# Kernel optimization log

Measured on AMD Instinct MI355X. Metric: run time of the kernel, lower is better.

Reference implementation:

```python
import jax, jax.numpy as jnp
from jax import lax
import numpy as np

N, T, HID, COMB, ATT, K, D = 128, 64, 512, 1024, 128, 20, 2
FMAP = 64  # CNN output channels; feature map is 14x14 -> 196 locations
ODIM = K + 2 * K * D + K + 1  # 121 mixture-density output params


def setup_inputs() -> dict:
    key = jax.random.key(0)
    keys = iter(jax.random.split(key, 64))

    def rn(shape, s=0.05):
        return jax.random.normal(next(keys), shape, jnp.float32) * s

    inp = dict(
        x=rn((N, T, D), 1.0),
        x_canv=jax.random.uniform(next(keys), (N, 1, 28, 28), dtype=jnp.float32),
        start=rn((N, D), 1.0),
        conv1_w=rn((16, 1, 3, 3), 0.3), conv1_b=rn((16,)),
        conv2_w=rn((32, 16, 3, 3), 0.1), conv2_b=rn((32,)),
        conv3_w=rn((64, 32, 3, 3), 0.1), conv3_b=rn((64,)),
        init_w=rn((2 * HID, FMAP + 16)), init_b=rn((2 * HID,)),
        Uw=rn((ATT, HID)), Ub=rn((ATT,)),
        Ww=rn((ATT, FMAP)), Wb=rn((ATT,)),
        vw=rn((1, ATT)), vb=rn((1,)),
        beta_w=rn((FMAP, HID)), beta_b=rn((FMAP,)),
        xemb_w=rn((16, D), 0.5), xemb_b=rn((16,)),
        semb_w=rn((16, D), 0.5), semb_b=rn((16,)),
        Wih=rn((4 * HID, FMAP + 16)), Whh=rn((4 * HID, HID)),
        bih=rn((4 * HID,)), bhh=rn((4 * HID,)),
        comb_w=rn((COMB, FMAP + HID + 32)), comb_b=rn((COMB,)),
        out_w=rn((ODIM, COMB)), out_b=rn((ODIM,)),
    )
    return inp


def _conv(x, w, b, stride):
    # torch Conv2d(kernel=3, padding=1) with NCHW / OIHW layout
    y = lax.conv_general_dilated(x, w, (stride, stride), ((1, 1), (1, 1)),
                                 dimension_numbers=('NCHW', 'OIHW', 'NCHW'))
    return y + b[None, :, None, None]


def reference(x, x_canv, start, conv1_w, conv1_b, conv2_w, conv2_b, conv3_w, conv3_b,
              init_w, init_b, Uw, Ub, Ww, Wb, vw, vb, beta_w, beta_b,
              xemb_w, xemb_b, semb_w, semb_b, Wih, Whh, bih, bhh,
              comb_w, comb_b, out_w, out_b):
    n, Tt, d = x.shape
    # sequence_pad: prepend zero vector, drop last step
    xp = jnp.concatenate([jnp.zeros((n, 1, d), x.dtype), x[:, :-1]], axis=1)
    xe = jnp.tanh(xp @ xemb_w.T + xemb_b)          # (n,T,16)
    se = jnp.tanh(start @ semb_w.T + semb_b)       # (n,16)
    # CNN (zscore_canvases with new_stats=True)
    c = (x_canv - 0.0243) / 0.1383
    c = jax.nn.relu(_conv(c, conv1_w, conv1_b, 1))
    c = jax.nn.relu(_conv(c, conv2_w, conv2_b, 1))
    c = jnp.tanh(_conv(c, conv3_w, conv3_b, 2))    # (n,64,14,14)
    a = c.transpose(0, 2, 3, 1).reshape(n, -1, FMAP)  # (n,196,64)
    # Initialize LSTM state (num_layers=1)
    hidden = jnp.tanh(jnp.concatenate([a.mean(axis=1), se], axis=1) @ init_w.T + init_b)
    hidden = hidden.reshape(n, HID, 2)
    h0, c0 = hidden[:, :, 0], hidden[:, :, 1]
    # AttendSAT.register_annotation: precompute W(a)
    W_a = a @ Ww.T + Wb                             # (n,196,att)
    # dropout masks are keep-probs (eval / dropout=0) -> all ones, identity

    def step(carry, xt):
        h, cs = carry
        Uh = h @ Uw.T + Ub                          # (n,att)
        e = (jnp.tanh(W_a + Uh[:, None, :]) @ vw.T).squeeze(-1) + vb[0]
        alpha = jax.nn.softmax(e, axis=-1)          # (n,196)
        z = jnp.einsum('nlf,nl->nf', a, alpha)      # (n,64)
        z = jax.nn.sigmoid(h @ beta_w.T + beta_b) * z
        gates = jnp.concatenate([xt, z], axis=1) @ Wih.T + bih + h @ Whh.T + bhh
        gi, gf, gg, go = jnp.split(gates, 4, axis=1)  # torch gate order i,f,g,o
        cs = jax.nn.sigmoid(gf) * cs + jax.nn.sigmoid(gi) * jnp.tanh(gg)
        h = jax.nn.sigmoid(go) * jnp.tanh(cs)
        y = jnp.tanh(jnp.concatenate([h, z, xt, se], axis=1) @ comb_w.T + comb_b)
        y = y @ out_w.T + out_b
        return (h, cs), y

    _, ys = lax.scan(step, (h0, c0), xe.transpose(1, 0, 2))
    y_out = ys.transpose(1, 0, 2)                   # (n,T,121)
    # unpack_output
    mix, means, scales, corrs, vlog = jnp.split(
        y_out, [K, K + K * D, K + 2 * K * D, 2 * K + 2 * K * D], axis=-1)
    mix = jax.nn.softmax(mix, axis=-1)
    means = means.reshape(n, Tt, K, D)
    scales = jnp.exp(scales).reshape(n, Tt, K, D)
    corrs = jnp.tanh(corrs)
    return (mix, means, scales, corrs, vlog.squeeze(-1))
```

## Files before the change

### kernel.cpp

```cpp
#include <hip/hip_runtime.h>


#define TN 128
#define TT 64

typedef __attribute__((ext_vector_type(4))) float f32x4;
typedef __attribute__((ext_vector_type(8))) short bf16x8;

__device__ __forceinline__ float fsigm(float x){ return __builtin_amdgcn_rcpf(1.0f + __expf(-x)); }
__device__ __forceinline__ float ftanh(float x){ return 1.0f - 2.0f*__builtin_amdgcn_rcpf(1.0f + __expf(2.0f*x)); }
__device__ __forceinline__ unsigned short f2bf(float f){
  unsigned int u = __float_as_uint(f);
  u += 0x7fffu + ((u >> 16) & 1u);
  return (unsigned short)(u >> 16);
}
__device__ __forceinline__ float b2f(unsigned short u){ return __uint_as_float(((unsigned)u)<<16); }

__global__ __launch_bounds__(256) void k_conv1(const float* __restrict__ xc, const float* __restrict__ w,
                                               const float* __restrict__ b, float* __restrict__ c1){
  int idx = blockIdx.x*256 + threadIdx.x;
  if (idx >= TN*16*784) return;
  int p = idx % 784, oc = (idx/784) & 15, n = idx/(784*16);
  int py = p/28, px = p%28;
  const float* src = xc + n*784;
  float acc = b[oc];
  #pragma unroll
  for (int ky=0;ky<3;ky++){
    int iy = py+ky-1; if (iy<0||iy>=28) continue;
    #pragma unroll
    for (int kx=0;kx<3;kx++){
      int ix = px+kx-1; if (ix<0||ix>=28) continue;
      acc += (src[iy*28+ix]-0.0243f)*(1.0f/0.1383f) * w[oc*9+ky*3+kx];
    }
  }
  c1[idx] = fmaxf(acc, 0.0f);
}

__global__ __launch_bounds__(256) void k_im2col2(const float* __restrict__ c1, unsigned short* __restrict__ a2){
  int idx = blockIdx.x*256 + threadIdx.x;
  int k = idx % 160, r = idx / 160;
  unsigned short v = 0;
  if (k < 144){
    int ic = k/9, rem = k - ic*9, ky = rem/3, kx = rem - ky*3;
    int p = r % 784, n = r / 784;
    int py = p/28, px = p%28;
    int iy = py+ky-1, ix = px+kx-1;
    if (iy>=0 && iy<28 && ix>=0 && ix<28) v = f2bf(c1[(n*16+ic)*784 + iy*28+ix]);
  }
  a2[idx] = v;
}

__global__ __launch_bounds__(256) void k_gconv2(const unsigned short* __restrict__ a2,
    const unsigned short* __restrict__ w2b, const float* __restrict__ b2,
    unsigned short* __restrict__ c2bf){
  int mbase = blockIdx.x*128;
  int tid = threadIdx.x, w = tid>>6, l = tid&63;
  int lr = l&15, lk = (l>>4)*8;
  __shared__ unsigned short at[128*168];
  {
    int row = tid>>1, off = (tid&1)*80;
    const unsigned short* sp = a2 + (size_t)(mbase+row)*160 + off;
    #pragma unroll
    for (int j=0;j<10;j++) *(float4*)&at[row*168 + off + j*8] = *(const float4*)(sp + j*8);
  }
  __syncthreads();
  f32x4 acc[2][2];
  #pragma unroll
  for (int mi=0;mi<2;mi++){ acc[mi][0]=(f32x4){0,0,0,0}; acc[mi][1]=(f32x4){0,0,0,0}; }
  for (int kt=0; kt<5; ++kt){
    bf16x8 b0 = *(const bf16x8*)(w2b + (0*16+lr)*160 + kt*32 + lk);
    bf16x8 b1 = *(const bf16x8*)(w2b + (1*16+lr)*160 + kt*32 + lk);
    #pragma unroll
    for (int mi=0;mi<2;mi++){
      bf16x8 afrag = *(const bf16x8*)&at[((2*w+mi)*16+lr)*168 + kt*32 + lk];
      acc[mi][0] = __builtin_amdgcn_mfma_f32_16x16x32_bf16(afrag, b0, acc[mi][0], 0,0,0);
      acc[mi][1] = __builtin_amdgcn_mfma_f32_16x16x32_bf16(afrag, b1, acc[mi][1], 0,0,0);
    }
  }
  #pragma unroll
  for (int mi=0;mi<2;mi++){
    #pragma unroll
    for (int j=0;j<2;j++){
      int oc = j*16 + lr;
      float bb = b2[oc];
      #pragma unroll
      for (int i=0;i<4;i++){
        int r = mbase + (2*w+mi)*16 + (l>>4)*4 + i;
        c2bf[(size_t)r*32 + oc] = f2bf(fmaxf(acc[mi][j][i] + bb, 0.0f));
      }
    }
  }
}

__global__ __launch_bounds__(256) void k_im2col3(const unsigned short* __restrict__ c2bf, unsigned short* __restrict__ a3){
  int idx = blockIdx.x*256 + threadIdx.x;
  int k = idx % 320, r = idx / 320;
  unsigned short v = 0;
  if (k < 288){
    int ic = k/9, rem = k - ic*9, ky = rem/3, kx = rem - ky*3;
    int p = r % 196, n = r / 196;
    int py = p/14, px = p%14;
    int iy = 2*py+ky-1, ix = 2*px+kx-1;
    if (iy>=0 && iy<28 && ix>=0 && ix<28) v = c2bf[(size_t)(n*784 + iy*28+ix)*32 + ic];
  }
  a3[idx] = v;
}

__global__ __launch_bounds__(256) void k_gconv3(const unsigned short* __restrict__ a3,
    const unsigned short* __restrict__ w3b, const float* __restrict__ b3,
    unsigned short* __restrict__ afbf, unsigned short* __restrict__ abf){
  int mbase = blockIdx.x*128;
  int tid = threadIdx.x, w = tid>>6, l = tid&63;
  int lr = l&15, lk = (l>>4)*8;
  __shared__ unsigned short at[128*168];
  f32x4 acc[2][4];
  #pragma unroll
  for (int mi=0;mi<2;mi++)
    #pragma unroll
    for (int j=0;j<4;j++) acc[mi][j]=(f32x4){0,0,0,0};
  for (int kt2=0; kt2<2; ++kt2){
    {
      int row = tid>>1, off = (tid&1)*80;
      const unsigned short* sp = a3 + (size_t)(mbase+row)*320 + kt2*160 + off;
      #pragma unroll
      for (int j=0;j<10;j++) *(float4*)&at[row*168 + off + j*8] = *(const float4*)(sp + j*8);
    }
    __syncthreads();
    for (int kt=0; kt<5; ++kt){
      #pragma unroll
      for (int mi=0;mi<2;mi++){
        bf16x8 afrag = *(const bf16x8*)&at[((2*w+mi)*16+lr)*168 + kt*32 + lk];
        #pragma unroll
        for (int j=0;j<4;j++){
          bf16x8 bf = *(const bf16x8*)(w3b + (size_t)(j*16+lr)*320 + kt2*160 + kt*32 + lk);
          acc[mi][j] = __builtin_amdgcn_mfma_f32_16x16x32_bf16(afrag, bf, acc[mi][j], 0,0,0);
        }
      }
    }
    __syncthreads();
  }
  #pragma unroll
  for (int mi=0;mi<2;mi++){
    #pragma unroll
    for (int j=0;j<4;j++){
      int oc = j*16 + lr;
      float bb = b3[oc];
      #pragma unroll
      for (int i=0;i<4;i++){
        int r = mbase + (2*w+mi)*16 + (l>>4)*4 + i;
        int n = r/196, p = r - n*196;
        float v = ftanh(acc[mi][j][i] + bb);
        unsigned short vb16 = f2bf(v);
        afbf[(size_t)(n*64+oc)*196 + p] = vb16;
        abf[(size_t)r*64 + oc] = vb16;
      }
    }
  }
}

__global__ __launch_bounds__(64) void k_amean(const unsigned short* __restrict__ afbf, float* __restrict__ amean){
  int n = blockIdx.x, f = threadIdx.x;
  const unsigned short* row = afbf + (size_t)(n*64+f)*196;
  float s = 0;
  for (int l=0;l<196;l++) s += b2f(row[l]);
  amean[n*64+f] = s * (1.0f/196.0f);
}

__global__ __launch_bounds__(256) void k_embed(const float* __restrict__ x, const float* __restrict__ start,
    const float* __restrict__ xw, const float* __restrict__ xb,
    const float* __restrict__ sw, const float* __restrict__ sb,
    float* __restrict__ xe, float* __restrict__ se){
  int idx = blockIdx.x*256 + threadIdx.x;
  if (idx < TN*TT*16){
    int j = idx & 15, t = (idx>>4) & 63, n = idx>>10;
    float acc = xb[j];
    if (t > 0){
      const float* xp = x + (n*TT + t-1)*2;
      acc += xp[0]*xw[j*2] + xp[1]*xw[j*2+1];
    }
    xe[idx] = ftanh(acc);
  } else if (idx < TN*TT*16 + TN*16){
    int k2 = idx - TN*TT*16;
    int j = k2 & 15, n = k2 >> 4;
    float acc = sb[j] + start[n*2]*sw[j*2] + start[n*2+1]*sw[j*2+1];
    se[k2] = ftanh(acc);
  }
}

__global__ __launch_bounds__(256) void k_init(const float* __restrict__ amean, const float* __restrict__ se,
    const float* __restrict__ w, const float* __restrict__ b,
    unsigned short* __restrict__ hbfA, float* __restrict__ cbuf){
  int idx = blockIdx.x*256 + threadIdx.x;
  if (idx >= TN*1024) return;
  int o = idx & 1023, n = idx >> 10;
  const float* wr = w + o*80;
  float acc = b[o];
  for (int k2=0;k2<64;k2++) acc += amean[n*64+k2]*wr[k2];
  for (int k2=0;k2<16;k2++) acc += se[n*16+k2]*wr[64+k2];
  float v = ftanh(acc);
  if (o & 1) cbuf[n*512 + (o>>1)] = v;
  else       hbfA[n*512 + (o>>1)] = f2bf(v);
}

__global__ __launch_bounds__(256) void k_prep(
    const float* __restrict__ Whh, const float* __restrict__ Wih,
    const float* __restrict__ bih, const float* __restrict__ bhh,
    const float* __restrict__ comb_w, const float* __restrict__ out_w, const float* __restrict__ out_b,
    const float* __restrict__ Uw, const float* __restrict__ beta_w, const float* __restrict__ Ww,
    const float* __restrict__ conv2_w, const float* __restrict__ conv3_w,
    unsigned short* __restrict__ wgf, float* __restrict__ gbias,
    unsigned short* __restrict__ cwbf, unsigned short* __restrict__ owbf, float* __restrict__ obias,
    unsigned short* __restrict__ uwbf, unsigned short* __restrict__ betabf, unsigned short* __restrict__ wwbf,
    unsigned short* __restrict__ w2b, unsigned short* __restrict__ w3b){
  int idx = blockIdx.x*256 + threadIdx.x;
  if (idx < 1245184){
    int fragi = idx >> 9;
    int lane8 = idx & 511;
    int lane = lane8 >> 3, j = lane8 & 7;
    int g = fragi / 608;
    int rem = fragi - g*608;
    int b = rem / 19, kt = rem - b*19;
    int row = g*512 + b*16 + (lane & 15);
    int col = kt*32 + (lane >> 4)*8 + j;
    float v = 0.f;
    if (col < 512) v = Whh[(size_t)row*512 + col];
    else { int c2 = col - 512; if (c2 < 80) v = Wih[(size_t)row*80 + c2]; }
    wgf[idx] = f2bf(v);
    return;
  }
  idx -= 1245184;
  if (idx < 2048){ gbias[idx] = bih[idx]+bhh[idx]; return; }
  idx -= 2048;
  if (idx < 622592){ cwbf[idx] = f2bf(comb_w[idx]); return; }
  idx -= 622592;
  if (idx < 131072){ int o = idx>>10, k2 = idx & 1023; owbf[idx] = (o<121)? f2bf(out_w[o*1024+k2]) : (unsigned short)0; return; }
  idx -= 131072;
  if (idx < 128){ obias[idx] = (idx<121)? out_b[idx] : 0.0f; return; }
  idx -= 128;
  if (idx < 65536){ uwbf[idx] = f2bf(Uw[idx]); return; }
  idx -= 65536;
  if (idx < 32768){ betabf[idx] = f2bf(beta_w[idx]); return; }
  idx -= 32768;
  if (idx < 8192){ wwbf[idx] = f2bf(Ww[idx]); return; }
  idx -= 8192;
  if (idx < 5120){ int o = idx/160, k2 = idx - o*160; w2b[idx] = (k2<144)? f2bf(conv2_w[o*144+k2]) : (unsigned short)0; return; }
  idx -= 5120;
  if (idx < 20480){ int o = idx/320, k2 = idx - o*320; w3b[idx] = (k2<288)? f2bf(conv3_w[o*320-o*320+o*320]) : (unsigned short)0;  }
  if (idx < 20480){ int o = idx/320, k2 = idx - o*320; w3b[idx] = (k2<288)? f2bf(conv3_w[o*288+k2]) : (unsigned short)0; return; }
}

__global__ __launch_bounds__(256) void k_wa(const unsigned short* __restrict__ abf,
    const unsigned short* __restrict__ wwbf, const float* __restrict__ Wb,
    unsigned short* __restrict__ wabf){
  int mbase = blockIdx.x*128;
  int tid = threadIdx.x, w = tid>>6, l = tid&63;
  int lr = l & 15, lk = (l>>4)*8;
  __shared__ unsigned short at[128*40];
  f32x4 acc[8][2];
  #pragma unroll
  for (int m=0;m<8;m++){ acc[m][0] = (f32x4){0,0,0,0}; acc[m][1] = (f32x4){0,0,0,0}; }
  for (int kt=0; kt<2; ++kt){
    int row = tid>>1, half = (tid&1)*16;
    const unsigned short* sp = abf + (mbase+row)*64 + kt*32 + half;
    *(float4*)&at[row*40 + half]     = *(const float4*)sp;
    *(float4*)&at[row*40 + half + 8] = *(const float4*)(sp + 8);
    __syncthreads();
    bf16x8 b0 = *(const bf16x8*)(wwbf + ((2*w+0)*16 + lr)*64 + kt*32 + lk);
    bf16x8 b1 = *(const bf16x8*)(wwbf + ((2*w+1)*16 + lr)*64 + kt*32 + lk);
    #pragma unroll
    for (int m=0;m<8;m++){
      bf16x8 afrag = *(const bf16x8*)&at[(m*16+lr)*40 + lk];
      acc[m][0] = __builtin_amdgcn_mfma_f32_16x16x32_bf16(afrag, b0, acc[m][0], 0,0,0);
      acc[m][1] = __builtin_amdgcn_mfma_f32_16x16x32_bf16(afrag, b1, acc[m][1], 0,0,0);
    }
    __syncthreads();
  }
  #pragma unroll
  for (int m=0;m<8;m++){
    #pragma unroll
    for (int j=0;j<2;j++){
      int att = (2*w+j)*16 + lr;
      float wb = Wb[att];
      #pragma unroll
      for (int i=0;i<4;i++){
        int arow = mbase + m*16 + (l>>4)*4 + i;
        int n = arow/196, l2 = arow - n*196;
        wabf[((size_t)n*196 + l2)*128 + att] = f2bf(acc[m][j][i] + wb);
      }
    }
  }
}

__global__ __launch_bounds__(512) void k_stepA(int t,
    const unsigned short* __restrict__ hbf_in,
    const unsigned short* __restrict__ uwbf, const float* __restrict__ Ub,
    const unsigned short* __restrict__ betabf, const float* __restrict__ beta_b,
    const float* __restrict__ vw, const float* __restrict__ vb,
    const unsigned short* __restrict__ wabf, const unsigned short* __restrict__ afbf,
    unsigned short* __restrict__ ubf_all, unsigned short* __restrict__ cbf,
    const unsigned short* __restrict__ wgf, float* __restrict__ gpart)
{
  const int bid = blockIdx.x, tid = threadIdx.x;
  __shared__ __align__(16) float hs[512];
  __shared__ __align__(16) float Uh[128];
  __shared__ __align__(16) float vws[128];
  __shared__ float bsig[64];
  __shared__ float ew[196];
  __shared__ float red[16];
  __shared__ float up[4][128];
  __shared__ float qp8[8][64];
  __shared__ float ep2[256][2];
  __shared__ __align__(16) unsigned short at2[2][128*36];

  if (bid < TN){
    const int n = bid;
    hs[tid] = b2f(hbf_in[n*512 + tid]);
    if (tid < 128) vws[tid] = vw[tid];
    const float vb0 = vb[0];
    __syncthreads();
    {
      int att = tid & 127, q = tid >> 7;
      const unsigned short* uw = uwbf + (size_t)att*512 + q*128;
      const float* hh = hs + q*128;
      float acc = 0.f;
      #pragma unroll 4
      for (int k=0;k<128;k+=8){
        bf16x8 v = *(const bf16x8*)(uw + k);
        acc += hh[k+0]*b2f(v[0]) + hh[k+1]*b2f(v[1]) + hh[k+2]*b2f(v[2]) + hh[k+3]*b2f(v[3])
             + hh[k+4]*b2f(v[4]) + hh[k+5]*b2f(v[5]) + hh[k+6]*b2f(v[6]) + hh[k+7]*b2f(v[7]);
      }
      up[q][att] = acc;
    }
    {
      int f = tid & 63, q = tid >> 6;
      const unsigned short* bw = betabf + (size_t)f*512 + q*64;
      const float* hh = hs + q*64;
      float acc = 0.f;
      #pragma unroll 4
      for (int k=0;k<64;k+=8){
        bf16x8 v = *(const bf16x8*)(bw + k);
        acc += hh[k+0]*b2f(v[0]) + hh[k+1]*b2f(v[1]) + hh[k+2]*b2f(v[2]) + hh[k+3]*b2f(v[3])
             + hh[k+4]*b2f(v[4]) + hh[k+5]*b2f(v[5]) + hh[k+6]*b2f(v[6]) + hh[k+7]*b2f(v[7]);
      }
      qp8[q][f] = acc;
    }
    __syncthreads();
    if (tid < 128) Uh[tid] = Ub[tid] + up[0][tid]+up[1][tid]+up[2][tid]+up[3][tid];
    else if (tid < 192){
      int f = tid-128;
      bsig[f] = fsigm(beta_b[f] + qp8[0][f]+qp8[1][f]+qp8[2][f]+qp8[3][f]
                                + qp8[4][f]+qp8[5][f]+qp8[6][f]+qp8[7][f]);
    }
    __syncthreads();
    {
      int l = tid >> 1, half = tid & 1;
      float acc = 0.f;
      if (l < 196){
        const unsigned short* wr = wabf + ((size_t)n*196 + l)*128 + half*64;
        const float* uh = Uh + half*64;
        const float* vv = vws + half*64;
        #pragma unroll 2
        for (int k=0;k<64;k+=8){
          bf16x8 wv = *(const bf16x8*)(wr + k);
          acc += vv[k+0]*ftanh(b2f(wv[0]) + uh[k+0]) + vv[k+1]*ftanh(b2f(wv[1]) + uh[k+1])
               + vv[k+2]*ftanh(b2f(wv[2]) + uh[k+2]) + vv[k+3]*ftanh(b2f(wv[3]) + uh[k+3])
               + vv[k+4]*ftanh(b2f(wv[4]) + uh[k+4]) + vv[k+5]*ftanh(b2f(wv[5]) + uh[k+5])
               + vv[k+6]*ftanh(b2f(wv[6]) + uh[k+6]) + vv[k+7]*ftanh(b2f(wv[7]) + uh[k+7]);
        }
      }
      ep2[l][half] = acc;
    }
    __syncthreads();
    float ev = -1e30f;
    if (tid < 196) ev = vb0 + ep2[tid][0] + ep2[tid][1];
    float m = ev;
    #pragma unroll
    for (int off=32; off>0; off>>=1) m = fmaxf(m, __shfl_xor(m, off));
    if ((tid&63)==0) red[tid>>6] = m;
    __syncthreads();
    float mx = red[0];
    #pragma unroll
    for (int i=1;i<8;i++) mx = fmaxf(mx, red[i]);
    float ex = (tid<196) ? __expf(ev - mx) : 0.0f;
    float ss = ex;
    #pragma unroll
    for (int off=32; off>0; off>>=1) ss += __shfl_xor(ss, off);
    if ((tid&63)==0) red[8+(tid>>6)] = ss;
    if (tid<196) ew[tid] = ex;
    __syncthreads();
    float inv = __builtin_amdgcn_rcpf(red[8]+red[9]+red[10]+red[11]+red[12]+red[13]+red[14]+red[15]);
    {
      int f = tid & 63, q = tid >> 6;
      int l0 = q*25, l1 = (l0+25 < 196) ? l0+25 : 196;
      const unsigned short* an = afbf + (size_t)n*12544 + (size_t)f*196;
      float acc = 0.f;
      for (int l2=l0; l2<l1; l2++) acc += ew[l2]*b2f(an[l2]);
      qp8[q][f] = acc;
    }
    __syncthreads();
    if (tid < 64){
      float z = bsig[tid]*(qp8[0][tid]+qp8[1][tid]+qp8[2][tid]+qp8[3][tid]
                          +qp8[4][tid]+qp8[5][tid]+qp8[6][tid]+qp8[7][tid])*inv;
      unsigned short zb = f2bf(z);
      ubf_all[((size_t)t*TN + n)*96 + 16 + tid] = zb;
      cbf[((size_t)n*TT + t)*608 + 512 + tid] = zb;
    }
  } else {
    const int b = bid - TN;
    const int w = tid>>6, l = tid&63, lr = l&15, li = l>>4, lk = li*8;
    const int g = w & 3, mh = w >> 2;
    bf16x8 wreg[16];
    {
      const unsigned short* wp = wgf + ((size_t)(g*32 + b)*19)*512 + (size_t)l*8;
      #pragma unroll
      for (int i=0;i<16;i++) wreg[i] = *(const bf16x8*)(wp + (size_t)i*512);
    }
    f32x4 acc[4];
    #pragma unroll
    for (int m2=0;m2<4;m2++) acc[m2] = (f32x4){0,0,0,0};
    {
      int row = tid>>2, seg = (tid&3)*8;
      *(float4*)&at2[0][row*36+seg] = *(const float4*)(hbf_in + (size_t)row*512 + seg);
    }
    __syncthreads();
    for (int kt=0; kt<16; ++kt){
      if (kt+1 < 16){
        int row = tid>>2, seg = (tid&3)*8;
        *(float4*)&at2[(kt+1)&1][row*36+seg] = *(const float4*)(hbf_in + (size_t)row*512 + (kt+1)*32 + seg);
      }
      #pragma unroll
      for (int m2=0;m2<4;m2++){
        bf16x8 a = *(const bf16x8*)&at2[kt&1][((mh*4+m2)*16 + lr)*36 + lk];
        acc[m2] = __builtin_amdgcn_mfma_f32_16x16x32_bf16(a, wreg[kt], acc[m2], 0,0,0);
      }
      __syncthreads();
    }
    #pragma unroll
    for (int m2=0;m2<4;m2++){
      #pragma unroll
      for (int i=0;i<4;i++){
        int n2 = (mh*4+m2)*16 + li*4 + i;
        gpart[(((size_t)g*128 + n2)<<9) + b*16 + lr] = acc[m2][i];
      }
    }
  }
}

__global__ __launch_bounds__(256) void k_stepB(int t,
    unsigned short* __restrict__ hout,
    const unsigned short* __restrict__ ubf_all,
    const unsigned short* __restrict__ wgf, const float* __restrict__ gbias,
    const float* __restrict__ gpart,
    float* __restrict__ cbuf, unsigned short* __restrict__ cbf)
{
  const int b = blockIdx.x, tid = threadIdx.x;
  const int w = tid>>6, l = tid&63, lr = l&15, li = l>>4, lk = li*8;
  __shared__ float gsh[4][128][16];
  __shared__ __align__(16) unsigned short at[128*100];
  const unsigned short* ub = ubf_all + (size_t)t*TN*96;
  for (int i = tid; i < 2048; i += 256){
    int g = i>>9, r = i&511, n2 = r>>2, j4 = r&3;
    *(float4*)&gsh[g][n2][j4*4] = *(const float4*)&gpart[(((size_t)g*128 + n2)<<9) + b*16 + j4*4];
  }
  for (int i = tid; i < 1536; i += 256){
    int row = i/12, c8 = i - row*12;
    *(float4*)&at[row*100 + c8*8] = *(const float4*)(ub + (size_t)row*96 + c8*8);
  }
  bf16x8 wz[3];
  {
    const unsigned short* wp = wgf + (((size_t)(w*32 + b)*19) + 16)*512 + (size_t)l*8;
    #pragma unroll
    for (int i=0;i<3;i++) wz[i] = *(const bf16x8*)(wp + (size_t)i*512);
  }
  f32x4 acc[8];
  #pragma unroll
  for (int m=0;m<8;m++) acc[m] = (f32x4){0,0,0,0};
  __syncthreads();
  #pragma unroll
  for (int kt=0; kt<3; ++kt){
    #pragma unroll
    for (int m=0;m<8;m++){
      bf16x8 a = *(const bf16x8*)&at[(m*16+lr)*100 + kt*32 + lk];
      acc[m] = __builtin_amdgcn_mfma_f32_16x16x32_bf16(a, wz[kt], acc[m], 0,0,0);
    }
  }
  #pragma unroll
  for (int m=0;m<8;m++)
    #pragma unroll
    for (int i=0;i<4;i++)
      gsh[w][m*16 + li*4 + i][lr] += acc[m][i];
  __syncthreads();
  #pragma unroll
  for (int e=0;e<8;++e){
    int c = tid*8 + e;
    int nn = c>>4, j = c&15;
    int hidx = b*16 + j;
    float gi = gsh[0][nn][j] + gbias[         hidx];
    float gf = gsh[1][nn][j] + gbias[1*512 + hidx];
    float gg = gsh[2][nn][j] + gbias[2*512 + hidx];
    float go = gsh[3][nn][j] + gbias[3*512 + hidx];
    float cc = cbuf[nn*512 + hidx];
    float cs = fsigm(gf)*cc + fsigm(gi)*ftanh(gg);
    float h  = fsigm(go)*ftanh(cs);
    cbuf[nn*512 + hidx] = cs;
    unsigned short hb = f2bf(h);
    hout[nn*512 + hidx] = hb;
    cbf[((size_t)nn*TT + t)*608 + hidx] = hb;
  }
}

__global__ __launch_bounds__(256) void k_cbf_xs(const float* __restrict__ xe, const float* __restrict__ se,
                                                unsigned short* __restrict__ cbf,
                                                unsigned short* __restrict__ ubf_all){
  int idx = blockIdx.x*256 + threadIdx.x;
  if (idx >= TN*TT*64) return;
  int j = idx & 63, r = idx >> 6;
  int n = r >> 6, t = r & 63;
  if (j < 16)      cbf[(size_t)r*608 + 576 + j] = f2bf(xe[r*16 + j]);
  else if (j < 32) cbf[(size_t)r*608 + 592 + (j-16)] = f2bf(se[n*16 + (j-16)]);
  else if (j < 48) ubf_all[((size_t)t*TN + n)*96 + (j-32)] = f2bf(xe[r*16 + (j-32)]);
  else             ubf_all[((size_t)t*TN + n)*96 + 80 + (j-48)] = 0;
}

__global__ __launch_bounds__(256) void k_comb(const unsigned short* __restrict__ cbf,
    const unsigned short* __restrict__ cwbf, const float* __restrict__ comb_b,
    unsigned short* __restrict__ ybf){
  int mbase = blockIdx.x*128, obase = blockIdx.y*128;
  int tid = threadIdx.x, w = tid>>6, l = tid&63;
  int lr = l&15, lk = (l>>4)*8;
  __shared__ unsigned short at[128*40];
  f32x4 acc[8][2];
  #pragma unroll
  for (int m=0;m<8;m++){ acc[m][0] = (f32x4){0,0,0,0}; acc[m][1] = (f32x4){0,0,0,0}; }
  for (int kt=0; kt<19; ++kt){
    int row = tid>>1, half = (tid&1)*16;
    const unsigned short* sp = cbf + (size_t)(mbase+row)*608 + kt*32 + half;
    *(float4*)&at[row*40 + half]     = *(const float4*)sp;
    *(float4*)&at[row*40 + half + 8] = *(const float4*)(sp + 8);
    __syncthreads();
    bf16x8 b0 = *(const bf16x8*)(cwbf + (size_t)(obase + (2*w+0)*16 + lr)*608 + kt*32 + lk);
    bf16x8 b1 = *(const bf16x8*)(cwbf + (size_t)(obase + (2*w+1)*16 + lr)*608 + kt*32 + lk);
    #pragma unroll
    for (int m=0;m<8;m++){
      bf16x8 afrag = *(const bf16x8*)&at[(m*16+lr)*40 + lk];
      acc[m][0] = __builtin_amdgcn_mfma_f32_16x16x32_bf16(afrag, b0, acc[m][0], 0,0,0);
      acc[m][1] = __builtin_amdgcn_mfma_f32_16x16x32_bf16(afrag, b1, acc[m][1], 0,0,0);
    }
    __syncthreads();
  }
  #pragma unroll
  for (int m=0;m<8;m++){
    #pragma unroll
    for (int j=0;j<2;j++){
      int o = obase + (2*w+j)*16 + lr;
      float cb = comb_b[o];
      #pragma unroll
      for (int i=0;i<4;i++){
        int r = mbase + m*16 + (l>>4)*4 + i;
        ybf[(size_t)r*1024 + o] = f2bf(ftanh(acc[m][j][i] + cb));
      }
    }
  }
}

__global__ __launch_bounds__(256) void k_out(const unsigned short* __restrict__ ybf,
    const unsigned short* __restrict__ owbf, const float* __restrict__ obias,
    float* __restrict__ obuf){
  int mbase = blockIdx.x*128;
  int tid = threadIdx.x, w = tid>>6, l = tid&63;
  int lr = l&15, lk = (l>>4)*8;
  __shared__ unsigned short at[128*40];
  f32x4 acc[8][2];
  #pragma unroll
  for (int m=0;m<8;m++){ acc[m][0] = (f32x4){0,0,0,0}; acc[m][1] = (f32x4){0,0,0,0}; }
  for (int kt=0; kt<32; ++kt){
    int row = tid>>1, half = (tid&1)*16;
    const unsigned short* sp = ybf + (size_t)(mbase+row)*1024 + kt*32 + half;
    *(float4*)&at[row*40 + half]     = *(const float4*)sp;
    *(float4*)&at[row*40 + half + 8] = *(const float4*)(sp + 8);
    __syncthreads();
    bf16x8 b0 = *(const bf16x8*)(owbf + ((2*w+0)*16 + lr)*1024 + kt*32 + lk);
    bf16x8 b1 = *(const bf16x8*)(owbf + ((2*w+1)*16 + lr)*1024 + kt*32 + lk);
    #pragma unroll
    for (int m=0;m<8;m++){
      bf16x8 afrag = *(const bf16x8*)&at[(m*16+lr)*40 + lk];
      acc[m][0] = __builtin_amdgcn_mfma_f32_16x16x32_bf16(afrag, b0, acc[m][0], 0,0,0);
      acc[m][1] = __builtin_amdgcn_mfma_f32_16x16x32_bf16(afrag, b1, acc[m][1], 0,0,0);
    }
    __syncthreads();
  }
  #pragma unroll
  for (int m=0;m<8;m++){
    #pragma unroll
    for (int j=0;j<2;j++){
      int o = (2*w+j)*16 + lr;
      float ob = obias[o];
      #pragma unroll
      for (int i=0;i<4;i++){
        int r = mbase + m*16 + (l>>4)*4 + i;
        obuf[(size_t)r*128 + o] = acc[m][j][i] + ob;
      }
    }
  }
}

__global__ __launch_bounds__(256) void k_post(const float* __restrict__ obuf, float* __restrict__ out){
  int r = blockIdx.x*256 + threadIdx.x;
  if (r >= TN*TT) return;
  const float* row = obuf + (size_t)r*128;
  float mx = -1e30f;
  #pragma unroll
  for (int k2=0;k2<20;k2++) mx = fmaxf(mx, row[k2]);
  float e[20]; float s = 0;
  #pragma unroll
  for (int k2=0;k2<20;k2++){ e[k2] = __expf(row[k2]-mx); s += e[k2]; }
  float inv = __builtin_amdgcn_rcpf(s);
  float* mixo  = out;
  float* meano = out + 163840;
  float* scaleo= out + 491520;
  float* corro = out + 819200;
  float* vlogo = out + 983040;
  #pragma unroll
  for (int k2=0;k2<20;k2++) mixo[r*20+k2] = e[k2]*inv;
  #pragma unroll
  for (int j=0;j<40;j++) meano[r*40+j] = row[20+j];
  #pragma unroll
  for (int j=0;j<40;j++) scaleo[r*40+j] = __expf(row[60+j]);
  #pragma unroll
  for (int k2=0;k2<20;k2++) corro[r*20+k2] = ftanh(row[100+k2]);
  vlogo[r] = row[120];
}

extern "C" void kernel_launch(void* const* d_in, const int* in_sizes, int n_in,
                              void* d_out, int out_size, void* d_ws, size_t ws_size,
                              hipStream_t stream){
  const float* x       = (const float*)d_in[0];
  const float* x_canv  = (const float*)d_in[1];
  const float* start_  = (const float*)d_in[2];
  const float* conv1_w = (const float*)d_in[3];
  const float* conv1_b = (const float*)d_in[4];
  const float* conv2_w = (const float*)d_in[5];
  const float* conv2_b = (const float*)d_in[6];
  const float* conv3_w = (const float*)d_in[7];
  const float* conv3_b = (const float*)d_in[8];
  const float* init_w  = (const float*)d_in[9];
  const float* init_b  = (const float*)d_in[10];
  const float* Uw      = (const float*)d_in[11];
  const float* Ub      = (const float*)d_in[12];
  const float* Ww      = (const float*)d_in[13];
  const float* Wb      = (const float*)d_in[14];
  const float* vw      = (const float*)d_in[15];
  const float* vb      = (const float*)d_in[16];
  const float* beta_w  = (const float*)d_in[17];
  const float* beta_b  = (const float*)d_in[18];
  const float* xemb_w  = (const float*)d_in[19];
  const float* xemb_b  = (const float*)d_in[20];
  const float* semb_w  = (const float*)d_in[21];
  const float* semb_b  = (const float*)d_in[22];
  const float* Wih     = (const float*)d_in[23];
  const float* Whh     = (const float*)d_in[24];
  const float* bih     = (const float*)d_in[25];
  const float* bhh     = (const float*)d_in[26];
  const float* comb_w  = (const float*)d_in[27];
  const float* comb_b  = (const float*)d_in[28];
  const float* out_w   = (const float*)d_in[29];
  const float* out_b   = (const float*)d_in[30];
  (void)in_sizes; (void)n_in; (void)out_size; (void)ws_size;

  char* wsb = (char*)d_ws;
  size_t off = 0;
  auto alloc = [&](size_t bytes)->char*{
    char* p = wsb + off;
    off = (off + bytes + 255) & ~(size_t)255;
    return p;
  };
  float*          c1     = (float*)alloc((size_t)TN*16*784*4);
  unsigned short* a2     = (unsigned short*)alloc((size_t)100352*160*2);
  unsigned short* a3     = a2;
  unsigned short* c2bf   = (unsigned short*)alloc((size_t)100352*32*2);
  unsigned short* afbf   = (unsigned short*)alloc((size_t)TN*64*196*2);
  unsigned short* abf    = (unsigned short*)alloc((size_t)TN*196*64*2);
  float*          amean  = (float*)alloc((size_t)TN*64*4);
  float*          xe     = (float*)alloc((size_t)TN*TT*16*4);
  float*          se     = (float*)alloc((size_t)TN*16*4);
  unsigned short* wabf   = (unsigned short*)alloc((size_t)TN*196*128*2);
  float*          cbuf   = (float*)alloc((size_t)TN*512*4);
  unsigned short* hbfA   = (unsigned short*)alloc((size_t)TN*512*2);
  unsigned short* hbfB   = (unsigned short*)alloc((size_t)TN*512*2);
  unsigned short* ubf_all= (unsigned short*)alloc((size_t)TT*TN*96*2);
  unsigned short* cbf    = (unsigned short*)alloc((size_t)TN*TT*608*2);
  unsigned short* ybf    = (unsigned short*)alloc((size_t)TN*TT*1024*2);
  float*          obuf   = (float*)alloc((size_t)TN*TT*128*4);
  unsigned short* wgf    = (unsigned short*)alloc((size_t)1245184*2);
  float*          gbias  = (float*)alloc((size_t)2048*4);
  float*          gpart  = (float*)alloc((size_t)4*128*512*4);
  unsigned short* cwbf   = (unsigned short*)alloc((size_t)1024*608*2);
  unsigned short* owbf   = (unsigned short*)alloc((size_t)128*1024*2);
  float*          obias  = (float*)alloc((size_t)128*4);
  unsigned short* uwbf   = (unsigned short*)alloc((size_t)128*512*2);
  unsigned short* betabf = (unsigned short*)alloc((size_t)64*512*2);
  unsigned short* wwbf   = (unsigned short*)alloc((size_t)128*64*2);
  unsigned short* w2b    = (unsigned short*)alloc((size_t)32*160*2);
  unsigned short* w3b    = (unsigned short*)alloc((size_t)64*320*2);

  hipLaunchKernelGGL(k_conv1, dim3(6272), dim3(256), 0, stream, x_canv, conv1_w, conv1_b, c1);
  hipLaunchKernelGGL(k_prep, dim3(8334), dim3(256), 0, stream,
                     Whh, Wih, bih, bhh, comb_w, out_w, out_b, Uw, beta_w, Ww, conv2_w, conv3_w,
                     wgf, gbias, cwbf, owbf, obias, uwbf, betabf, wwbf, w2b, w3b);
  hipLaunchKernelGGL(k_im2col2, dim3(62720), dim3(256), 0, stream, c1, a2);
  hipLaunchKernelGGL(k_gconv2, dim3(784), dim3(256), 0, stream, a2, w2b, conv2_b, c2bf);
  hipLaunchKernelGGL(k_im2col3, dim3(31360), dim3(256), 0, stream, c2bf, a3);
  hipLaunchKernelGGL(k_gconv3, dim3(196), dim3(256), 0, stream, a3, w3b, conv3_b, afbf, abf);
  hipLaunchKernelGGL(k_amean, dim3(128), dim3(64), 0, stream, afbf, amean);
  hipLaunchKernelGGL(k_embed, dim3(520), dim3(256), 0, stream, x, start_, xemb_w, xemb_b, semb_w, semb_b, xe, se);
  hipLaunchKernelGGL(k_init, dim3(512), dim3(256), 0, stream, amean, se, init_w, init_b, hbfA, cbuf);
  hipLaunchKernelGGL(k_wa, dim3(196), dim3(256), 0, stream, abf, wwbf, Wb, wabf);
  hipLaunchKernelGGL(k_cbf_xs, dim3(2048), dim3(256), 0, stream, xe, se, cbf, ubf_all);

  for (int t = 0; t < TT; ++t){
    unsigned short* hin  = (t & 1) ? hbfB : hbfA;
    unsigned short* hout = (t & 1) ? hbfA : hbfB;
    hipLaunchKernelGGL(k_stepA, dim3(160), dim3(512), 0, stream, t,
                       hin, uwbf, Ub, betabf, beta_b, vw, vb, wabf, afbf, ubf_all, cbf, wgf, gpart);
    hipLaunchKernelGGL(k_stepB, dim3(32), dim3(256), 0, stream, t,
                       hout, ubf_all, wgf, gbias, gpart, cbuf, cbf);
  }

  hipLaunchKernelGGL(k_comb, dim3(64, 8), dim3(256), 0, stream, cbf, cwbf, comb_b, ybf);
  hipLaunchKernelGGL(k_out, dim3(64), dim3(256), 0, stream, ybf, owbf, obias, obuf);
  hipLaunchKernelGGL(k_post, dim3(32), dim3(256), 0, stream, obuf, (float*)d_out);
}
```

Before: 1.670 ms.

## Store conv1 as bf16, read MFMA operands from global, widen stepB to 512 threads

conv1 now writes its output as bf16, which halves the traffic into im2col2 and drops a conversion there. In the recurrent kernels, the MFMA A operand (h and the u inputs) is loaded straight from global memory instead of being staged through double-buffered shared memory, which removes the per-iteration barriers. k_stepB goes from 256 to 512 threads, so each wave covers half the rows, following the same split as stepA's gate blocks. A stray duplicate store in the weight-prep kernel is also removed. The direct global loads depend on L2 and cache hits and are less coalesced than the staged path.

New measurement: 2.193 ms. +31.4%, slower.

```diff
diff --git a/kernel.cpp b/kernel.cpp
--- a/kernel.cpp
+++ b/kernel.cpp
@@ -17,7 +17,7 @@
 __device__ __forceinline__ float b2f(unsigned short u){ return __uint_as_float(((unsigned)u)<<16); }
 
 __global__ __launch_bounds__(256) void k_conv1(const float* __restrict__ xc, const float* __restrict__ w,
-                                               const float* __restrict__ b, float* __restrict__ c1){
+                                               const float* __restrict__ b, unsigned short* __restrict__ c1bf){
   int idx = blockIdx.x*256 + threadIdx.x;
   if (idx >= TN*16*784) return;
   int p = idx % 784, oc = (idx/784) & 15, n = idx/(784*16);
@@ -33,10 +33,10 @@
       acc += (src[iy*28+ix]-0.0243f)*(1.0f/0.1383f) * w[oc*9+ky*3+kx];
     }
   }
-  c1[idx] = fmaxf(acc, 0.0f);
-}
-
-__global__ __launch_bounds__(256) void k_im2col2(const float* __restrict__ c1, unsigned short* __restrict__ a2){
+  c1bf[idx] = f2bf(fmaxf(acc, 0.0f));
+}
+
+__global__ __launch_bounds__(256) void k_im2col2(const unsigned short* __restrict__ c1bf, unsigned short* __restrict__ a2){
   int idx = blockIdx.x*256 + threadIdx.x;
   int k = idx % 160, r = idx / 160;
   unsigned short v = 0;
@@ -45,7 +45,7 @@
     int p = r % 784, n = r / 784;
     int py = p/28, px = p%28;
     int iy = py+ky-1, ix = px+kx-1;
-    if (iy>=0 && iy<28 && ix>=0 && ix<28) v = f2bf(c1[(n*16+ic)*784 + iy*28+ix]);
+    if (iy>=0 && iy<28 && ix>=0 && ix<28) v = c1bf[(n*16+ic)*784 + iy*28+ix];
   }
   a2[idx] = v;
 }
@@ -245,7 +245,6 @@
   idx -= 8192;
   if (idx < 5120){ int o = idx/160, k2 = idx - o*160; w2b[idx] = (k2<144)? f2bf(conv2_w[o*144+k2]) : (unsigned short)0; return; }
   idx -= 5120;
-  if (idx < 20480){ int o = idx/320, k2 = idx - o*320; w3b[idx] = (k2<288)? f2bf(conv3_w[o*320-o*320+o*320]) : (unsigned short)0;  }
   if (idx < 20480){ int o = idx/320, k2 = idx - o*320; w3b[idx] = (k2<288)? f2bf(conv3_w[o*288+k2]) : (unsigned short)0; return; }
 }
 
@@ -310,7 +309,6 @@
   __shared__ float up[4][128];
   __shared__ float qp8[8][64];
   __shared__ float ep2[256][2];
-  __shared__ __align__(16) unsigned short at2[2][128*36];
 
   if (bid < TN){
     const int n = bid;
@@ -418,22 +416,13 @@
     f32x4 acc[4];
     #pragma unroll
     for (int m2=0;m2<4;m2++) acc[m2] = (f32x4){0,0,0,0};
-    {
-      int row = tid>>2, seg = (tid&3)*8;
-      *(float4*)&at2[0][row*36+seg] = *(const float4*)(hbf_in + (size_t)row*512 + seg);
-    }
-    __syncthreads();
+    #pragma unroll 4
     for (int kt=0; kt<16; ++kt){
-      if (kt+1 < 16){
-        int row = tid>>2, seg = (tid&3)*8;
-        *(float4*)&at2[(kt+1)&1][row*36+seg] = *(const float4*)(hbf_in + (size_t)row*512 + (kt+1)*32 + seg);
-      }
       #pragma unroll
       for (int m2=0;m2<4;m2++){
-        bf16x8 a = *(const bf16x8*)&at2[kt&1][((mh*4+m2)*16 + lr)*36 + lk];
+        bf16x8 a = *(const bf16x8*)(hbf_in + (size_t)((mh*4+m2)*16 + lr)*512 + kt*32 + lk);
         acc[m2] = __builtin_amdgcn_mfma_f32_16x16x32_bf16(a, wreg[kt], acc[m2], 0,0,0);
       }
-      __syncthreads();
     }
     #pragma unroll
     for (int m2=0;m2<4;m2++){
@@ -446,7 +435,7 @@
   }
 }
 
-__global__ __launch_bounds__(256) void k_stepB(int t,
+__global__ __launch_bounds__(512) void k_stepB(int t,
     unsigned short* __restrict__ hout,
     const unsigned short* __restrict__ ubf_all,
     const unsigned short* __restrict__ wgf, const float* __restrict__ gbias,
@@ -455,44 +444,40 @@
 {
   const int b = blockIdx.x, tid = threadIdx.x;
   const int w = tid>>6, l = tid&63, lr = l&15, li = l>>4, lk = li*8;
+  const int g = w & 3, mh = w >> 2;
   __shared__ float gsh[4][128][16];
-  __shared__ __align__(16) unsigned short at[128*100];
   const unsigned short* ub = ubf_all + (size_t)t*TN*96;
-  for (int i = tid; i < 2048; i += 256){
-    int g = i>>9, r = i&511, n2 = r>>2, j4 = r&3;
-    *(float4*)&gsh[g][n2][j4*4] = *(const float4*)&gpart[(((size_t)g*128 + n2)<<9) + b*16 + j4*4];
-  }
-  for (int i = tid; i < 1536; i += 256){
-    int row = i/12, c8 = i - row*12;
-    *(float4*)&at[row*100 + c8*8] = *(const float4*)(ub + (size_t)row*96 + c8*8);
-  }
   bf16x8 wz[3];
   {
-    const unsigned short* wp = wgf + (((size_t)(w*32 + b)*19) + 16)*512 + (size_t)l*8;
+    const unsigned short* wp = wgf + (((size_t)(g*32 + b)*19) + 16)*512 + (size_t)l*8;
     #pragma unroll
     for (int i=0;i<3;i++) wz[i] = *(const bf16x8*)(wp + (size_t)i*512);
   }
-  f32x4 acc[8];
-  #pragma unroll
-  for (int m=0;m<8;m++) acc[m] = (f32x4){0,0,0,0};
+  for (int i = tid; i < 2048; i += 512){
+    int gg = i>>9, r = i&511, n2 = r>>2, j4 = r&3;
+    *(float4*)&gsh[gg][n2][j4*4] = *(const float4*)&gpart[(((size_t)gg*128 + n2)<<9) + b*16 + j4*4];
+  }
+  f32x4 acc[4];
+  #pragma unroll
+  for (int m2=0;m2<4;m2++) acc[m2] = (f32x4){0,0,0,0};
+  #pragma unroll
+  for (int kt=0; kt<3; ++kt){
+    #pragma unroll
+    for (int m2=0;m2<4;m2++){
+      bf16x8 a = *(const bf16x8*)(ub + (size_t)((mh*4+m2)*16 + lr)*96 + kt*32 + lk);
+      acc[m2] = __builtin_amdgcn_mfma_f32_16x16x32_bf16(a, wz[kt], acc[m2], 0,0,0);
+    }
+  }
   __syncthreads();
   #pragma unroll
-  for (int kt=0; kt<3; ++kt){
-    #pragma unroll
-    for (int m=0;m<8;m++){
-      bf16x8 a = *(const bf16x8*)&at[(m*16+lr)*100 + kt*32 + lk];
-      acc[m] = __builtin_amdgcn_mfma_f32_16x16x32_bf16(a, wz[kt], acc[m], 0,0,0);
-    }
-  }
-  #pragma unroll
-  for (int m=0;m<8;m++)
+  for (int m2=0;m2<4;m2++)
     #pragma unroll
     for (int i=0;i<4;i++)
-      gsh[w][m*16 + li*4 + i][lr] += acc[m][i];
+      gsh[g][(mh*4+m2)*16 + li*4 + i][lr] += acc[m2][i];
   __syncthreads();
   #pragma unroll
-  for (int e=0;e<8;++e){
-    int c = tid*8 + e;
+  for (int e=0;e<4;++e){
+    int c = tid*4 + e;
     int nn = c>>4, j = c&15;
     int hidx = b*16 + j;
     float gi = gsh[0][nn][j] + gbias[         hidx];
@@ -674,7 +659,7 @@
     off = (off + bytes + 255) & ~(size_t)255;
     return p;
   };
-  float*          c1     = (float*)alloc((size_t)TN*16*784*4);
+  unsigned short* c1bf   = (unsigned short*)alloc((size_t)TN*16*784*2);
   unsigned short* a2     = (unsigned short*)alloc((size_t)100352*160*2);
   unsigned short* a3     = a2;
   unsigned short* c2bf   = (unsigned short*)alloc((size_t)100352*32*2);
@@ -703,11 +688,11 @@
   unsigned short* w2b    = (unsigned short*)alloc((size_t)32*160*2);
   unsigned short* w3b    = (unsigned short*)alloc((size_t)64*320*2);
 
-  hipLaunchKernelGGL(k_conv1, dim3(6272), dim3(256), 0, stream, x_canv, conv1_w, conv1_b, c1);
+  hipLaunchKernelGGL(k_conv1, dim3(6272), dim3(256), 0, stream, x_canv, conv1_w, conv1_b, c1bf);
   hipLaunchKernelGGL(k_prep, dim3(8334), dim3(256), 0, stream,
                      Whh, Wih, bih, bhh, comb_w, out_w, out_b, Uw, beta_w, Ww, conv2_w, conv3_w,
                      wgf, gbias, cwbf, owbf, obias, uwbf, betabf, wwbf, w2b, w3b);
-  hipLaunchKernelGGL(k_im2col2, dim3(62720), dim3(256), 0, stream, c1, a2);
+  hipLaunchKernelGGL(k_im2col2, dim3(62720), dim3(256), 0, stream, c1bf, a2);
   hipLaunchKernelGGL(k_gconv2, dim3(784), dim3(256), 0, stream, a2, w2b, conv2_b, c2bf);
   hipLaunchKernelGGL(k_im2col3, dim3(31360), dim3(256), 0, stream, c2bf, a3);
   hipLaunchKernelGGL(k_gconv3, dim3(196), dim3(256), 0, stream, a3, w3b, conv3_b, afbf, abf);
@@ -722,7 +707,7 @@
     unsigned short* hout = (t & 1) ? hbfA : hbfB;
     hipLaunchKernelGGL(k_stepA, dim3(160), dim3(512), 0, stream, t,
                        hin, uwbf, Ub, betabf, beta_b, vw, vb, wabf, afbf, ubf_all, cbf, wgf, gpart);
-    hipLaunchKernelGGL(k_stepB, dim3(32), dim3(256), 0, stream, t,
+    hipLaunchKernelGGL(k_stepB, dim3(32), dim3(512), 0, stream, t,
                        hout, ubf_all, wgf, gbias, gpart, cbuf, cbf);
   }
 
```
